# Kernel optimization log

Hardware: AMD Instinct MI355X
Metric: run time of the kernel (lower is better)

The kernel has to match this reference:

```python
import jax, jax.numpy as jnp
import numpy as np

NUM_HEADS = 12
LOCAL_WINDOW = 7


def setup_inputs() -> dict:
    key = jax.random.key(0)
    k1, k2, k3 = jax.random.split(key, 3)
    B, N, C = 2, 2048, 768
    x = jax.random.normal(k1, (B, N, C), dtype=jnp.float32)
    w_qkv = jax.random.normal(k2, (3 * C, C), dtype=jnp.float32) * (C ** -0.5)
    w_proj = jax.random.normal(k3, (C, C), dtype=jnp.float32) * (C ** -0.5)
    b_proj = jnp.zeros((C,), dtype=jnp.float32)
    return {"x": x, "w_qkv": w_qkv, "w_proj": w_proj, "b_proj": b_proj}


def reference(x, w_qkv, w_proj, b_proj):
    B, N, C = x.shape
    H = NUM_HEADS
    Dh = C // H
    scale = Dh ** -0.5
    # local-window additive mask: 0 within |i-j|<=w, -inf outside (vectorized)
    idx = jnp.arange(N)
    local_mask = jnp.where(
        jnp.abs(idx[:, None] - idx[None, :]) <= LOCAL_WINDOW, 0.0, -jnp.inf
    ).astype(x.dtype)
    qkv = x @ w_qkv.T
    qkv = qkv.reshape(B, N, 3, H, Dh).transpose(2, 0, 3, 1, 4)
    q, k, v = qkv[0], qkv[1], qkv[2]
    attn = jnp.einsum("bhnd,bhmd->bhnm", q, k) * scale
    attn = attn + local_mask[None, None, :, :]
    attn = jax.nn.softmax(attn, axis=-1)
    out = jnp.einsum("bhnm,bhmd->bhnd", attn, v)
    out = out.transpose(0, 2, 1, 3).reshape(B, N, C)
    return out @ w_proj.T + b_proj
```

## Files before the change

kernel.cpp:

```cpp
#include <hip/hip_runtime.h>
#include <hip/hip_bf16.h>

typedef __bf16 bf16;
typedef bf16 bf16x4 __attribute__((ext_vector_type(4)));
typedef bf16 bf16x8 __attribute__((ext_vector_type(8)));
typedef float floatx4 __attribute__((ext_vector_type(4)));

#define GLOBAL_AS __attribute__((address_space(1)))
#define LDS_AS __attribute__((address_space(3)))

__device__ __forceinline__ void hard_barrier() {
    asm volatile("" ::: "memory");
    __builtin_amdgcn_s_barrier();
    asm volatile("" ::: "memory");
}

__global__ __launch_bounds__(256)
void cvt3_f32_bf16(const float* __restrict__ s0, const float* __restrict__ s1,
                   const float* __restrict__ s2, bf16* __restrict__ d0,
                   bf16* __restrict__ d1, bf16* __restrict__ d2,
                   int n0, int n1, int n2)
{
    int t = blockIdx.x * blockDim.x + threadIdx.x;
    const float* s; bf16* d; int i;
    if (t < n0)                { s = s0; d = d0; i = t; }
    else if (t < n0 + n1)      { s = s1; d = d1; i = t - n0; }
    else if (t < n0 + n1 + n2) { s = s2; d = d2; i = t - n0 - n1; }
    else return;
    float4 v = ((const float4*)s)[i];
    bf16x4 o = { (bf16)v.x, (bf16)v.y, (bf16)v.z, (bf16)v.w };
    ((bf16x4*)d)[i] = o;
}

template<typename CT, int M, int N, int K, int LDA, int LDC>
__global__ __launch_bounds__(512, 2)
void gemm8p_bt(const bf16* __restrict__ A, const bf16* __restrict__ W,
               CT* __restrict__ C)
{
    constexpr int NT = K / 64;
    __shared__ __align__(16) bf16 lds[2][(256 + 192) * 64];

    const int tid  = threadIdx.x;
    const int lane = tid & 63;
    const int wave = tid >> 6;

    int lin = blockIdx.x;
    const int chx = gridDim.x >> 3;
    lin = (lin & 7) * chx + (lin >> 3);
    const int bx = lin / (N / 192);
    const int by = lin % (N / 192);
    const int row0 = bx * 256;
    const int col0 = by * 192;

    const int wm = (wave & 1) * 128;
    const int wn = (wave >> 1) * 48;

    const int fr  = lane & 15;
    const int fks = lane >> 4;
    const int fr7 = fr & 7;

    const int rl = tid >> 3;
    const int sl = tid & 7;
    const int ss = sl ^ (rl & 7);

    floatx4 acc[8][3] = {};

    auto stageA = [&](int k0, bf16* Ld) {
        #pragma unroll
        for (int c = 0; c < 4; ++c) {
            const bf16* src = A + (size_t)(row0 + c * 64 + rl) * LDA + k0 + ss * 8;
            __builtin_amdgcn_global_load_lds((const GLOBAL_AS void*)src,
                (LDS_AS void*)(Ld + c * 4096 + wave * 512), 16, 0, 0);
        }
    };
    auto stageB = [&](int k0, bf16* Ld) {
        #pragma unroll
        for (int c = 0; c < 3; ++c) {
            const bf16* src = W + (size_t)(col0 + c * 64 + rl) * K + k0 + ss * 8;
            __builtin_amdgcn_global_load_lds((const GLOBAL_AS void*)src,
                (LDS_AS void*)(Ld + c * 4096 + wave * 512), 16, 0, 0);
        }
    };

    bf16x8 afA[4][2], b01[2][2], b2[1][2];

    auto loadA = [&](const bf16* Ab, int qi) {
        #pragma unroll
        for (int ii = 0; ii < 4; ++ii)
            #pragma unroll
            for (int kk = 0; kk < 2; ++kk)
                afA[ii][kk] = *(const bf16x8*)(Ab
                    + (wm + (qi + ii) * 16 + fr) * 64
                    + (((kk * 4 + fks) ^ fr7) * 8));
    };
    auto loadB01 = [&](const bf16* Bb) {
        #pragma unroll
        for (int jj = 0; jj < 2; ++jj)
            #pragma unroll
            for (int kk = 0; kk < 2; ++kk)
                b01[jj][kk] = *(const bf16x8*)(Bb
                    + (wn + jj * 16 + fr) * 64
                    + (((kk * 4 + fks) ^ fr7) * 8));
    };
    auto loadB2 = [&](const bf16* Bb) {
        #pragma unroll
        for (int kk = 0; kk < 2; ++kk)
            b2[0][kk] = *(const bf16x8*)(Bb
                + (wn + 2 * 16 + fr) * 64
                + (((kk * 4 + fks) ^ fr7) * 8));
    };
    auto mfma16 = [&](int qi) {
        __builtin_amdgcn_s_setprio(1);
        #pragma unroll
        for (int ii = 0; ii < 4; ++ii)
            #pragma unroll
            for (int jj = 0; jj < 2; ++jj)
                #pragma unroll
                for (int kk = 0; kk < 2; ++kk)
                    acc[qi + ii][jj] = __builtin_amdgcn_mfma_f32_16x16x32_bf16(
                        afA[ii][kk], b01[jj][kk], acc[qi + ii][jj], 0, 0, 0);
        __builtin_amdgcn_s_setprio(0);
        hard_barrier();
    };
    auto mfma8 = [&](int qi) {
        __builtin_amdgcn_s_setprio(1);
        #pragma unroll
        for (int ii = 0; ii < 4; ++ii)
            #pragma unroll
            for (int kk = 0; kk < 2; ++kk)
                acc[qi + ii][2] = __builtin_amdgcn_mfma_f32_16x16x32_bf16(
                    afA[ii][kk], b2[0][kk], acc[qi + ii][2], 0, 0, 0);
        __builtin_amdgcn_s_setprio(0);
        hard_barrier();
    };

    stageA(0, lds[0]);
    stageB(0, lds[0] + 256 * 64);

    for (int t = 0; t < NT; ++t) {
        const int buf = t & 1;
        const bf16* Ab = lds[buf];
        const bf16* Bb = lds[buf] + 256 * 64;
        asm volatile("s_waitcnt lgkmcnt(0)" ::: "memory");
        if (t + 1 < NT) {
            stageA((t + 1) * 64, lds[buf ^ 1]);
            stageB((t + 1) * 64, lds[buf ^ 1] + 256 * 64);
            asm volatile("s_waitcnt vmcnt(7)" ::: "memory");
        } else {
            asm volatile("s_waitcnt vmcnt(0)" ::: "memory");
        }
        hard_barrier();

        loadA(Ab, 0);
        loadB01(Bb);
        loadB2(Bb);
        mfma16(0);
        mfma8(0);
        loadA(Ab, 4);
        mfma8(4);
        mfma16(4);
    }

    const int fc  = lane & 15;
    const int fr4 = (lane >> 4) * 4;
    #pragma unroll
    for (int i = 0; i < 8; ++i)
        #pragma unroll
        for (int j = 0; j < 3; ++j) {
            const int col = col0 + wn + j * 16 + fc;
            #pragma unroll
            for (int r = 0; r < 4; ++r) {
                const int row = row0 + wm + i * 16 + fr4 + r;
                C[(size_t)row * LDC + col] = (CT)acc[i][j][r];
            }
        }
}

template<typename CT, int TM, int M, int N, int K, int LDA, int LDC>
__global__ __launch_bounds__(256, 2)
void gemm_bt_p(const bf16* __restrict__ A, const bf16* __restrict__ W,
               CT* __restrict__ C, const float* __restrict__ bias)
{
    constexpr int MI  = TM / 32;
    constexpr int CAW = TM / 64;
    constexpr int NT  = K / 32;
    __shared__ __align__(16) bf16 As[2][TM * 32];
    __shared__ __align__(16) bf16 Bs[2][128 * 32];

    const int tid  = threadIdx.x;
    const int lane = tid & 63;
    const int wave = tid >> 6;

    const int lin = blockIdx.y * gridDim.x + blockIdx.x;
    const int ch  = gridDim.x >> 3;
    const int xcd = lin & 7;
    const int rr  = lin >> 3;
    const int bx  = xcd * ch + (rr % ch);
    const int by  = rr / ch;

    const int row0 = bx * TM;
    const int col0 = by * 128;

    const int wm = (wave & 1) * (TM / 2);
    const int wn = (wave >> 1) * 64;

    floatx4 acc[MI][4] = {};

    const int fr = lane & 15;
    const int fk = (lane >> 4) * 8;

    const int lr = lane >> 2;
    const int lk = (lane & 3) * 8;

    auto stage = [&](int k0, int buf) {
        #pragma unroll
        for (int c = 0; c < CAW; ++c) {
            const int chunk = wave * CAW + c;
            const int r = chunk * 16 + lr;
            const bf16* gA = A + (size_t)(row0 + r) * LDA + k0 + lk;
            __builtin_amdgcn_global_load_lds((const GLOBAL_AS void*)gA,
                                             (LDS_AS void*)(As[buf] + chunk * 512),
                                             16, 0, 0);
        }
        #pragma unroll
        for (int c = 0; c < 2; ++c) {
            const int chunk = wave * 2 + c;
            const int r = chunk * 16 + lr;
            const bf16* gB = W + (size_t)(col0 + r) * K + k0 + lk;
            __builtin_amdgcn_global_load_lds((const GLOBAL_AS void*)gB,
                                             (LDS_AS void*)(Bs[buf] + chunk * 512),
                                             16, 0, 0);
        }
    };

    stage(0, 0);
    for (int t = 0; t < NT; ++t) {
        const int buf = t & 1;
        if (t + 1 < NT) {
            stage((t + 1) * 32, buf ^ 1);
            if (TM == 64) asm volatile("s_waitcnt vmcnt(3)" ::: "memory");
            else          asm volatile("s_waitcnt vmcnt(4)" ::: "memory");
        } else {
            asm volatile("s_waitcnt vmcnt(0)" ::: "memory");
        }
        hard_barrier();

        bf16x8 af[MI], bfr[4];
        #pragma unroll
        for (int i = 0; i < MI; ++i)
            af[i]  = *(const bf16x8*)(As[buf] + (wm + i * 16 + fr) * 32 + fk);
        #pragma unroll
        for (int j = 0; j < 4; ++j)
            bfr[j] = *(const bf16x8*)(Bs[buf] + (wn + j * 16 + fr) * 32 + fk);
        #pragma unroll
        for (int i = 0; i < MI; ++i)
            #pragma unroll
            for (int j = 0; j < 4; ++j)
                acc[i][j] = __builtin_amdgcn_mfma_f32_16x16x32_bf16(
                    af[i], bfr[j], acc[i][j], 0, 0, 0);

        asm volatile("s_waitcnt lgkmcnt(0)" ::: "memory");
        hard_barrier();
    }

    const int fc  = lane & 15;
    const int fr4 = (lane >> 4) * 4;
    #pragma unroll
    for (int i = 0; i < MI; ++i) {
        #pragma unroll
        for (int j = 0; j < 4; ++j) {
            const int col = col0 + wn + j * 16 + fc;
            const float b = bias ? bias[col] : 0.0f;
            #pragma unroll
            for (int r = 0; r < 4; ++r) {
                const int row = row0 + wm + i * 16 + fr4 + r;
                C[(size_t)row * LDC + col] = (CT)(acc[i][j][r] + b);
            }
        }
    }
}

template<typename CT, bool AF32, bool WF32, int TM, int M, int N, int K,
         int LDA, int LDC>
__global__ __launch_bounds__(256, 2)
void gemm_bt(const void* __restrict__ Av, const void* __restrict__ Wv,
             CT* __restrict__ C, const float* __restrict__ bias)
{
    constexpr int MI = TM / 32;
    __shared__ __align__(16) bf16 As[TM * 32];
    __shared__ __align__(16) bf16 Bs[128 * 32];

    const int tid  = threadIdx.x;
    const int lane = tid & 63;
    const int wave = tid >> 6;

    const int lin = blockIdx.y * gridDim.x + blockIdx.x;
    const int ch  = gridDim.x >> 3;
    const int xcd = lin & 7;
    const int rr  = lin >> 3;
    const int bx  = xcd * ch + (rr % ch);
    const int by  = rr / ch;

    const int row0 = bx * TM;
    const int col0 = by * 128;

    const int wm = (wave & 1) * (TM / 2);
    const int wn = (wave >> 1) * 64;

    floatx4 acc[MI][4] = {};

    const int fr = lane & 15;
    const int fk = (lane >> 4) * 8;

    const int lr = lane >> 2;
    const int lk = (lane & 3) * 8;

    for (int k0 = 0; k0 < K; k0 += 32) {
        if (AF32) {
            constexpr int NV = TM * 4;
            #pragma unroll
            for (int c = 0; c < NV / 256; ++c) {
                const int idx = tid + c * 256;
                const int r   = idx >> 2;
                const int cb  = (idx & 3) * 8;
                const float4* g = (const float4*)((const float*)Av
                                   + (size_t)(row0 + r) * LDA + k0 + cb);
                float4 g0 = g[0], g1 = g[1];
                bf16x8 va;
                va[0]=(bf16)g0.x; va[1]=(bf16)g0.y; va[2]=(bf16)g0.z; va[3]=(bf16)g0.w;
                va[4]=(bf16)g1.x; va[5]=(bf16)g1.y; va[6]=(bf16)g1.z; va[7]=(bf16)g1.w;
                *(bf16x8*)(As + r * 32 + cb) = va;
            }
        } else {
            constexpr int CAW = TM / 64;
            #pragma unroll
            for (int c = 0; c < CAW; ++c) {
                const int chunk = wave * CAW + c;
                const int r = chunk * 16 + lr;
                const bf16* gA = (const bf16*)Av + (size_t)(row0 + r) * LDA + k0 + lk;
                __builtin_amdgcn_global_load_lds((const GLOBAL_AS void*)gA,
                                                 (LDS_AS void*)(As + chunk * 512),
                                                 16, 0, 0);
            }
        }
        if (WF32) {
            #pragma unroll
            for (int c = 0; c < 2; ++c) {
                const int idx = tid + c * 256;
                const int r   = idx >> 2;
                const int cb  = (idx & 3) * 8;
                const float4* g = (const float4*)((const float*)Wv
                                   + (size_t)(col0 + r) * K + k0 + cb);
                float4 g0 = g[0], g1 = g[1];
                bf16x8 vw;
                vw[0]=(bf16)g0.x; vw[1]=(bf16)g0.y; vw[2]=(bf16)g0.z; vw[3]=(bf16)g0.w;
                vw[4]=(bf16)g1.x; vw[5]=(bf16)g1.y; vw[6]=(bf16)g1.z; vw[7]=(bf16)g1.w;
                *(bf16x8*)(Bs + r * 32 + cb) = vw;
            }
        } else {
            #pragma unroll
            for (int c = 0; c < 2; ++c) {
                const int chunk = wave * 2 + c;
                const int r = chunk * 16 + lr;
                const bf16* gB = (const bf16*)Wv + (size_t)(col0 + r) * K + k0 + lk;
                __builtin_amdgcn_global_load_lds((const GLOBAL_AS void*)gB,
                                                 (LDS_AS void*)(Bs + chunk * 512),
                                                 16, 0, 0);
            }
        }
        __syncthreads();

        bf16x8 af[MI], bfr[4];
        #pragma unroll
        for (int i = 0; i < MI; ++i)
            af[i]  = *(const bf16x8*)(As + (wm + i * 16 + fr) * 32 + fk);
        #pragma unroll
        for (int j = 0; j < 4; ++j)
            bfr[j] = *(const bf16x8*)(Bs + (wn + j * 16 + fr) * 32 + fk);
        #pragma unroll
        for (int i = 0; i < MI; ++i)
            #pragma unroll
            for (int j = 0; j < 4; ++j)
                acc[i][j] = __builtin_amdgcn_mfma_f32_16x16x32_bf16(
                    af[i], bfr[j], acc[i][j], 0, 0, 0);

        __syncthreads();
    }

    const int fc  = lane & 15;
    const int fr4 = (lane >> 4) * 4;
    #pragma unroll
    for (int i = 0; i < MI; ++i) {
        #pragma unroll
        for (int j = 0; j < 4; ++j) {
            const int col = col0 + wn + j * 16 + fc;
            const float b = bias ? bias[col] : 0.0f;
            #pragma unroll
            for (int r = 0; r < 4; ++r) {
                const int row = row0 + wm + i * 16 + fr4 + r;
                C[(size_t)row * LDC + col] = (CT)(acc[i][j][r] + b);
            }
        }
    }
}

__global__ __launch_bounds__(256)
void attn_tile(const bf16* __restrict__ qkv, bf16* __restrict__ aout)
{
    __shared__ __align__(16) bf16 Vt[4][64][40];
    __shared__ __align__(16) bf16 Ps[4][16][40];

    const int w    = threadIdx.x >> 6;
    const int lane = threadIdx.x & 63;
    const int c    = lane & 15;
    const int q    = lane >> 4;
    int bid = blockIdx.x;
    bid = (bid & 7) * 96 + (bid >> 3);
    const int wid  = bid * 4 + w;
    const int it   = wid & 127;
    const int bh   = wid >> 7;
    const int h    = bh % 12;
    const int b    = bh / 12;
    const int I0   = it * 16;
    const int bbase = b * 2048;
    const int j0   = I0 - 7;

    #pragma unroll
    for (int itr = 0; itr < 4; ++itr) {
        int idx = itr * 64 + lane;
        int row = idx >> 3;
        int dc  = (idx & 7) * 8;
        int jc  = j0 + row; jc = jc < 0 ? 0 : (jc > 2047 ? 2047 : jc);
        const bf16* base = qkv + (size_t)(bbase + jc) * 2304 + 1536 + h * 64 + dc;
        bf16x8 vv = *(const bf16x8*)base;
        #pragma unroll
        for (int e = 0; e < 8; ++e) {
            int d    = dc + e;
            int col2 = (row * 2) ^ (((d >> 3) & 3) << 4);
            *(bf16*)((char*)&Vt[w][d][0] + col2) = vv[e];
        }
    }

    const bf16* qrow = qkv + (size_t)(bbase + I0 + c) * 2304 + h * 64;
    bf16x8 aq0 = *(const bf16x8*)(qrow + q * 8);
    bf16x8 aq1 = *(const bf16x8*)(qrow + 32 + q * 8);

    floatx4 st[2] = {};
    #pragma unroll
    for (int t = 0; t < 2; ++t) {
        int jr = j0 + t * 16 + c;
        jr = jr < 0 ? 0 : (jr > 2047 ? 2047 : jr);
        const bf16* krow = qkv + (size_t)(bbase + jr) * 2304 + 768 + h * 64;
        bf16x8 k0 = *(const bf16x8*)(krow + q * 8);
        bf16x8 k1 = *(const bf16x8*)(krow + 32 + q * 8);
        st[t] = __builtin_amdgcn_mfma_f32_16x16x32_bf16(aq0, k0, st[t], 0, 0, 0);
        st[t] = __builtin_amdgcn_mfma_f32_16x16x32_bf16(aq1, k1, st[t], 0, 0, 0);
    }

    float s[2][4];
    #pragma unroll
    for (int t = 0; t < 2; ++t)
        #pragma unroll
        for (int r = 0; r < 4; ++r) {
            int il = q * 4 + r;
            int jl = t * 16 + c;
            int ja = j0 + jl;
            bool valid = (jl >= il) && (jl <= il + 14) && (ja >= 0) && (ja < 2048);
            s[t][r] = valid ? st[t][r] * 0.125f : -1e30f;
        }

    float l[4], p[2][4];
    #pragma unroll
    for (int r = 0; r < 4; ++r) {
        float m2 = fmaxf(s[0][r], s[1][r]);
        #pragma unroll
        for (int mk = 1; mk < 16; mk <<= 1) m2 = fmaxf(m2, __shfl_xor(m2, mk, 64));
        p[0][r] = __expf(s[0][r] - m2);
        p[1][r] = __expf(s[1][r] - m2);
        float l2 = p[0][r] + p[1][r];
        #pragma unroll
        for (int mk = 1; mk < 16; mk <<= 1) l2 += __shfl_xor(l2, mk, 64);
        l[r] = l2;
    }

    #pragma unroll
    for (int r = 0; r < 4; ++r) {
        Ps[w][q * 4 + r][c]      = (bf16)p[0][r];
        Ps[w][q * 4 + r][16 + c] = (bf16)p[1][r];
    }

    bf16x8 ap = *(const bf16x8*)(&Ps[w][c][q * 8]);
    floatx4 ov[4];
    #pragma unroll
    for (int nt = 0; nt < 4; ++nt) {
        int dr = nt * 16 + c;
        int cb = (q * 16) ^ (((dr >> 3) & 3) << 4);
        bf16x8 vf = *(const bf16x8*)((const char*)&Vt[w][dr][0] + cb);
        floatx4 z = {};
        ov[nt] = __builtin_amdgcn_mfma_f32_16x16x32_bf16(ap, vf, z, 0, 0, 0);
    }

    float rl[4];
    #pragma unroll
    for (int r = 0; r < 4; ++r) rl[r] = 1.0f / l[r];
    #pragma unroll
    for (int r = 0; r < 4; ++r) {
        bf16* orow = aout + (size_t)(bbase + I0 + q * 4 + r) * 768 + h * 64;
        #pragma unroll
        for (int nt = 0; nt < 4; ++nt)
            orow[nt * 16 + c] = (bf16)(ov[nt][r] * rl[r]);
    }
}

extern "C" void kernel_launch(void* const* d_in, const int* in_sizes, int n_in,
                              void* d_out, int out_size, void* d_ws, size_t ws_size,
                              hipStream_t stream)
{
    const float* x      = (const float*)d_in[0];
    const float* w_qkv  = (const float*)d_in[1];
    const float* w_proj = (const float*)d_in[2];
    const float* b_proj = (const float*)d_in[3];
    float* out = (float*)d_out;

    bf16* qkv = (bf16*)d_ws;
    const size_t QKV_B  = (size_t)4096 * 2304 * 2;
    const size_t AO_B   = (size_t)4096 * 768 * 2;
    const size_t XB_B   = (size_t)4096 * 768 * 2;
    const size_t WQKV_B = (size_t)2304 * 768 * 2;
    const size_t WPRJ_B = (size_t)768 * 768 * 2;

    if (ws_size >= QKV_B + AO_B + XB_B + WQKV_B + WPRJ_B) {
        bf16* aout = (bf16*)((char*)d_ws + QKV_B);
        bf16* xb   = (bf16*)((char*)aout + AO_B);
        bf16* wqb  = (bf16*)((char*)xb + XB_B);
        bf16* wpb  = (bf16*)((char*)wqb + WQKV_B);

        const int n0 = 4096 * 768 / 4, n1 = 2304 * 768 / 4, n2 = 768 * 768 / 4;
        cvt3_f32_bf16<<<dim3((n0 + n1 + n2) / 256), 256, 0, stream>>>(
            x, w_qkv, w_proj, xb, wqb, wpb, n0, n1, n2);

        gemm8p_bt<bf16, 4096, 2304, 768, 768, 2304>
            <<<dim3(192), 512, 0, stream>>>(xb, wqb, qkv);

        attn_tile<<<dim3(768), 256, 0, stream>>>(qkv, aout);

        gemm_bt_p<float, 64, 4096, 768, 768, 768, 768>
            <<<dim3(64, 6), 256, 0, stream>>>(aout, wpb, out, b_proj);
    } else {
        gemm_bt<bf16, true, true, 128, 4096, 2304, 768, 768, 2304>
            <<<dim3(32, 18), 256, 0, stream>>>(x, w_qkv, qkv, nullptr);

        bf16* aout = (bf16*)((char*)d_ws + QKV_B);
        attn_tile<<<dim3(768), 256, 0, stream>>>(qkv, aout);

        gemm_bt<float, false, true, 64, 4096, 768, 768, 768, 768>
            <<<dim3(64, 6), 256, 0, stream>>>(aout, w_proj, out, b_proj);
    }
}
```

Baseline: 118.7 us.

## Replace output projection GEMM with 128x128 8-wave kernel using swizzled LDS

The output projection GEMM now uses 128x128 tiles with 8 waves, K-step 64, XOR-swizzled LDS layout, XCD-aware block remapping, and MFMA phases wrapped in s_setprio. This replaces the 64x128 tile, 4-wave, K-step 32 kernel. The aim is more data reuse per tile, fewer LDS bank conflicts and fewer barrier iterations. The trade-off is only 192 blocks (fewer than the previous 384) and more LDS per block, which can hurt occupancy and tail balance on a small GEMM.

```diff
diff --git a/kernel.cpp b/kernel.cpp
--- a/kernel.cpp
+++ b/kernel.cpp
@@ -176,99 +176,119 @@
         }
 }
 
-template<typename CT, int TM, int M, int N, int K, int LDA, int LDC>
-__global__ __launch_bounds__(256, 2)
-void gemm_bt_p(const bf16* __restrict__ A, const bf16* __restrict__ W,
-               CT* __restrict__ C, const float* __restrict__ bias)
+template<typename CT, int M, int N, int K, int LDA, int LDC>
+__global__ __launch_bounds__(512, 2)
+void gemm8p2_bt(const bf16* __restrict__ A, const bf16* __restrict__ W,
+                CT* __restrict__ C, const float* __restrict__ bias)
 {
-    constexpr int MI  = TM / 32;
-    constexpr int CAW = TM / 64;
-    constexpr int NT  = K / 32;
-    __shared__ __align__(16) bf16 As[2][TM * 32];
-    __shared__ __align__(16) bf16 Bs[2][128 * 32];
+    constexpr int NT = K / 64;
+    __shared__ __align__(16) bf16 lds[2][(128 + 128) * 64];
 
     const int tid  = threadIdx.x;
     const int lane = tid & 63;
     const int wave = tid >> 6;
 
-    const int lin = blockIdx.y * gridDim.x + blockIdx.x;
-    const int ch  = gridDim.x >> 3;
-    const int xcd = lin & 7;
-    const int rr  = lin >> 3;
-    const int bx  = xcd * ch + (rr % ch);
-    const int by  = rr / ch;
-
-    const int row0 = bx * TM;
+    int lin = blockIdx.x;
+    const int chx = gridDim.x >> 3;
+    lin = (lin & 7) * chx + (lin >> 3);
+    const int bx = lin / (N / 128);
+    const int by = lin % (N / 128);
+    const int row0 = bx * 128;
     const int col0 = by * 128;
 
-    const int wm = (wave & 1) * (TM / 2);
-    const int wn = (wave >> 1) * 64;
-
-    floatx4 acc[MI][4] = {};
-
-    const int fr = lane & 15;
-    const int fk = (lane >> 4) * 8;
-
-    const int lr = lane >> 2;
-    const int lk = (lane & 3) * 8;
-
-    auto stage = [&](int k0, int buf) {
-        #pragma unroll
-        for (int c = 0; c < CAW; ++c) {
-            const int chunk = wave * CAW + c;
-            const int r = chunk * 16 + lr;
-            const bf16* gA = A + (size_t)(row0 + r) * LDA + k0 + lk;
-            __builtin_amdgcn_global_load_lds((const GLOBAL_AS void*)gA,
-                                             (LDS_AS void*)(As[buf] + chunk * 512),
-                                             16, 0, 0);
-        }
+    const int wm = (wave & 1) * 64;
+    const int wn = (wave >> 1) * 32;
+
+    const int fr  = lane & 15;
+    const int fks = lane >> 4;
+    const int fr7 = fr & 7;
+
+    const int rl = tid >> 3;
+    const int sl = tid & 7;
+    const int ss = sl ^ (rl & 7);
+
+    floatx4 acc[4][2] = {};
+
+    auto stageA = [&](int k0, bf16* Ld) {
         #pragma unroll
         for (int c = 0; c < 2; ++c) {
-            const int chunk = wave * 2 + c;
-            const int r = chunk * 16 + lr;
-            const bf16* gB = W + (size_t)(col0 + r) * K + k0 + lk;
-            __builtin_amdgcn_global_load_lds((const GLOBAL_AS void*)gB,
-                                             (LDS_AS void*)(Bs[buf] + chunk * 512),
-                                             16, 0, 0);
-        }
-    };
-
-    stage(0, 0);
+            const bf16* src = A + (size_t)(row0 + c * 64 + rl) * LDA + k0 + ss * 8;
+            __builtin_amdgcn_global_load_lds((const GLOBAL_AS void*)src,
+                (LDS_AS void*)(Ld + c * 4096 + wave * 512), 16, 0, 0);
+        }
+    };
+    auto stageB = [&](int k0, bf16* Ld) {
+        #pragma unroll
+        for (int c = 0; c < 2; ++c) {
+            const bf16* src = W + (size_t)(col0 + c * 64 + rl) * K + k0 + ss * 8;
+            __builtin_amdgcn_global_load_lds((const GLOBAL_AS void*)src,
+                (LDS_AS void*)(Ld + c * 4096 + wave * 512), 16, 0, 0);
+        }
+    };
+
+    bf16x8 afA[4][2], bb[2][2];
+
+    auto loadA = [&](const bf16* Ab) {
+        #pragma unroll
+        for (int ii = 0; ii < 4; ++ii)
+            #pragma unroll
+            for (int kk = 0; kk < 2; ++kk)
+                afA[ii][kk] = *(const bf16x8*)(Ab
+                    + (wm + ii * 16 + fr) * 64
+                    + (((kk * 4 + fks) ^ fr7) * 8));
+    };
+    auto loadB = [&](const bf16* Bb) {
+        #pragma unroll
+        for (int jj = 0; jj < 2; ++jj)
+            #pragma unroll
+            for (int kk = 0; kk < 2; ++kk)
+                bb[jj][kk] = *(const bf16x8*)(Bb
+                    + (wn + jj * 16 + fr) * 64
+                    + (((kk * 4 + fks) ^ fr7) * 8));
+    };
+    auto mfmaH = [&](int qi) {
+        __builtin_amdgcn_s_setprio(1);
+        #pragma unroll
+        for (int ii = 0; ii < 2; ++ii)
+            #pragma unroll
+            for (int jj = 0; jj < 2; ++jj)
+                #pragma unroll
+                for (int kk = 0; kk < 2; ++kk)
+                    acc[qi + ii][jj] = __builtin_amdgcn_mfma_f32_16x16x32_bf16(
+                        afA[qi + ii][kk], bb[jj][kk], acc[qi + ii][jj], 0, 0, 0);
+        __builtin_amdgcn_s_setprio(0);
+        hard_barrier();
+    };
+
+    stageA(0, lds[0]);
+    stageB(0, lds[0] + 128 * 64);
+
     for (int t = 0; t < NT; ++t) {
         const int buf = t & 1;
+        const bf16* Ab = lds[buf];
+        const bf16* Bb = lds[buf] + 128 * 64;
+        asm volatile("s_waitcnt lgkmcnt(0)" ::: "memory");
         if (t + 1 < NT) {
-            stage((t + 1) * 32, buf ^ 1);
-            if (TM == 64) asm volatile("s_waitcnt vmcnt(3)" ::: "memory");
-            else          asm volatile("s_waitcnt vmcnt(4)" ::: "memory");
+            stageA((t + 1) * 64, lds[buf ^ 1]);
+            stageB((t + 1) * 64, lds[buf ^ 1] + 128 * 64);
+            asm volatile("s_waitcnt vmcnt(4)" ::: "memory");
         } else {
             asm volatile("s_waitcnt vmcnt(0)" ::: "memory");
         }
         hard_barrier();
 
-        bf16x8 af[MI], bfr[4];
-        #pragma unroll
-        for (int i = 0; i < MI; ++i)
-            af[i]  = *(const bf16x8*)(As[buf] + (wm + i * 16 + fr) * 32 + fk);
-        #pragma unroll
-        for (int j = 0; j < 4; ++j)
-            bfr[j] = *(const bf16x8*)(Bs[buf] + (wn + j * 16 + fr) * 32 + fk);
-        #pragma unroll
-        for (int i = 0; i < MI; ++i)
-            #pragma unroll
-            for (int j = 0; j < 4; ++j)
-                acc[i][j] = __builtin_amdgcn_mfma_f32_16x16x32_bf16(
-                    af[i], bfr[j], acc[i][j], 0, 0, 0);
-
-        asm volatile("s_waitcnt lgkmcnt(0)" ::: "memory");
-        hard_barrier();
+        loadA(Ab);
+        loadB(Bb);
+        mfmaH(0);
+        mfmaH(2);
     }
 
     const int fc  = lane & 15;
     const int fr4 = (lane >> 4) * 4;
     #pragma unroll
-    for (int i = 0; i < MI; ++i) {
-        #pragma unroll
-        for (int j = 0; j < 4; ++j) {
+    for (int i = 0; i < 4; ++i)
+        #pragma unroll
+        for (int j = 0; j < 2; ++j) {
             const int col = col0 + wn + j * 16 + fc;
             const float b = bias ? bias[col] : 0.0f;
             #pragma unroll
@@ -277,7 +297,6 @@
                 C[(size_t)row * LDC + col] = (CT)(acc[i][j][r] + b);
             }
         }
-    }
 }
 
 template<typename CT, bool AF32, bool WF32, int TM, int M, int N, int K,
@@ -544,8 +563,8 @@
 
         attn_tile<<<dim3(768), 256, 0, stream>>>(qkv, aout);
 
-        gemm_bt_p<float, 64, 4096, 768, 768, 768, 768>
-            <<<dim3(64, 6), 256, 0, stream>>>(aout, wpb, out, b_proj);
+        gemm8p2_bt<float, 4096, 768, 768, 768, 768>
+            <<<dim3(192), 512, 0, stream>>>(aout, wpb, out, b_proj);
     } else {
         gemm_bt<bf16, true, true, 128, 4096, 2304, 768, 768, 2304>
             <<<dim3(32, 18), 256, 0, stream>>>(x, w_qkv, qkv, nullptr);
```

Result: faster. 115.4 us (-2.8%).
